# Kernel tuning notes

Measured on AMD Instinct MI355X. Metric: run time of the kernel, lower is better.

The kernel has to match this reference:

```python
import jax, jax.numpy as jnp
from jax import lax
import numpy as np

STATE_DIM, H, L = 38000, 32, 3
B, T = 256, 1024


def setup_inputs() -> dict:
    key = jax.random.key(0)
    ks = jax.random.split(key, 16)
    s = 1.0 / np.sqrt(H)
    inp = {
        "x": jax.random.randint(ks[0], (B, T), 0, STATE_DIM, dtype=jnp.int64)
        if jax.config.jax_enable_x64 else jax.random.randint(ks[0], (B, T), 0, STATE_DIM, dtype=jnp.int32),
        "hid": jnp.zeros((L, B, H), dtype=jnp.float32),
        "emb": jax.random.normal(ks[1], (STATE_DIM, H), dtype=jnp.float32),
        "W1": jax.random.uniform(ks[2], (H, H), minval=-s, maxval=s),
        "b1": jax.random.uniform(ks[3], (H,), minval=-s, maxval=s),
        "W2": jax.random.uniform(ks[4], (H, H), minval=-s, maxval=s),
        "b2": jax.random.uniform(ks[5], (H,), minval=-s, maxval=s),
        "W3": jax.random.uniform(ks[6], (H, H), minval=-s, maxval=s),
        "b3": jax.random.uniform(ks[7], (H,), minval=-s, maxval=s),
        # GRU params stacked over layers: gates order (r, z, n) as in PyTorch
        "W_ih": jax.random.uniform(ks[8], (L, 3 * H, H), minval=-s, maxval=s),
        "W_hh": jax.random.uniform(ks[9], (L, 3 * H, H), minval=-s, maxval=s),
        "b_ih": jax.random.uniform(ks[10], (L, 3 * H), minval=-s, maxval=s),
        "b_hh": jax.random.uniform(ks[11], (L, 3 * H), minval=-s, maxval=s),
    }
    return inp


def _gru_layer(x_tbh, h0, W_ih, W_hh, b_ih, b_hh):
    # x_tbh: [T,B,H]; precompute input-side gates once (memory-bound GEMM)
    gi = jnp.einsum('tbh,gh->tbg', x_tbh, W_ih) + b_ih  # [T,B,3H]

    def step(h, gi_t):
        gh = h @ W_hh.T + b_hh  # [B,3H]
        i_r, i_z, i_n = jnp.split(gi_t, 3, axis=-1)
        h_r, h_z, h_n = jnp.split(gh, 3, axis=-1)
        r = jax.nn.sigmoid(i_r + h_r)
        z = jax.nn.sigmoid(i_z + h_z)
        n = jnp.tanh(i_n + r * h_n)
        h_new = (1.0 - z) * n + z * h
        return h_new, h_new

    hT, out = lax.scan(step, h0, gi)
    return out, hT  # [T,B,H], [B,H]


def reference(x, hid, emb, W1, b1, W2, b2, W3, b3, W_ih, W_hh, b_ih, b_hh):
    e = emb[x]  # [B,T,H] embedding lookup
    e = jax.nn.relu(e @ W1.T + b1)
    e = jax.nn.relu(e @ W2.T + b2)
    e = jax.nn.relu(e @ W3.T + b3)
    seq = jnp.transpose(e, (1, 0, 2))  # [T,B,H]
    h_finals = []
    for l in range(L):
        seq, hT = _gru_layer(seq, hid[l], W_ih[l], W_hh[l], b_ih[l], b_hh[l])
        h_finals.append(hT)
    out = jnp.transpose(seq, (1, 0, 2)).reshape(x.shape[0], -1)  # [B, T*H]
    return out, jnp.stack(h_finals, axis=0)
```

## Files before the change

### kernel.cpp

```cpp
#include <hip/hip_runtime.h>

#define BB 256
#define TT 1024
#define HH 32
#define SS 16
#define NBK (TT/SS)
#define NSS (NBK+9)
#define NT 1024
#define SP 32
#define GP 96


__device__ __forceinline__ float fast_rcp(float x) { return __builtin_amdgcn_rcpf(x); }
__device__ __forceinline__ float sigm(float x)     { return fast_rcp(1.f + __expf(-x)); }
__device__ __forceinline__ float tanh_fast(float x){ float e = __expf(2.f * x); return 1.f - 2.f * fast_rcp(e + 1.f); }
__device__ __forceinline__ float rlane(float v, int k) {
    return __int_as_float(__builtin_amdgcn_readlane(__float_as_int(v), k));
}

__global__ __launch_bounds__(NT, 4) void rnn_fused(
    const int*   __restrict__ xidx,
    const float* __restrict__ hid,
    const float* __restrict__ emb,
    const float* __restrict__ W1, const float* __restrict__ b1,
    const float* __restrict__ W2, const float* __restrict__ b2,
    const float* __restrict__ W3, const float* __restrict__ b3,
    const float* __restrict__ Wih,
    const float* __restrict__ Whh,
    const float* __restrict__ bih,
    const float* __restrict__ bhh,
    float*       __restrict__ out)
{
    const int b   = blockIdx.x;
    const int tid = threadIdx.x;
    const int wv  = tid >> 6;
    const int ln  = tid & 63;
    const int lo  = ln & 31;
    const int hh  = ln >> 5;

    __shared__ alignas(16) float ebuf[2][SS][SP];
    __shared__ alignas(16) float y1s [2][SS][SP];
    __shared__ alignas(16) float y2s [2][SS][SP];
    __shared__ alignas(16) float y3s [2][SS][SP];
    __shared__ alignas(16) float h0s [2][SS][SP];
    __shared__ alignas(16) float h1s [2][SS][SP];
    __shared__ alignas(16) float gib [3][2][SS][GP];

    float wA[32], wB[32];
    float biasA = 0.f, biasB = 0.f, v_h = 0.f;

    if (wv < 3) {
        const float4* pA = reinterpret_cast<const float4*>(Whh + (size_t)(wv * 96 + ln) * HH);
        const float4* pB = reinterpret_cast<const float4*>(Whh + (size_t)(wv * 96 + 64 + lo) * HH);
        #pragma unroll
        for (int i = 0; i < 8; ++i) {
            reinterpret_cast<float4*>(wA)[i] = pA[i];
            reinterpret_cast<float4*>(wB)[i] = pB[i];
        }
        biasA = bhh[wv * 96 + ln];
        biasB = bhh[wv * 96 + 64 + lo];
        if (ln < HH) v_h = hid[(size_t)(wv * BB + b) * HH + ln];
    } else if (wv < 6) {
        const int l = wv - 3;
        const float4* pA = reinterpret_cast<const float4*>(Wih + (size_t)(l * 96 + ln) * HH);
        #pragma unroll
        for (int i = 0; i < 8; ++i) reinterpret_cast<float4*>(wA)[i] = pA[i];
        biasA = bih[l * 96 + ln];
    } else if (wv < 9) {
        const int l = wv - 6;
        const float4* pA = reinterpret_cast<const float4*>(Wih + (size_t)(l * 96 + 64 + lo) * HH);
        #pragma unroll
        for (int i = 0; i < 8; ++i) reinterpret_cast<float4*>(wA)[i] = pA[i];
        biasA = bih[l * 96 + 64 + lo];
    } else if (wv < 12) {
        const float* Ws = (wv == 9) ? W1 : (wv == 10) ? W2 : W3;
        const float* bs = (wv == 9) ? b1 : (wv == 10) ? b2 : b3;
        const float4* pA = reinterpret_cast<const float4*>(Ws + (size_t)lo * HH);
        #pragma unroll
        for (int i = 0; i < 8; ++i) reinterpret_cast<float4*>(wA)[i] = pA[i];
        biasA = bs[lo];
    }
    __syncthreads();

    float* const out_seq = out + (size_t)b * TT * HH;
    float* const out_hf  = out + (size_t)BB * TT * HH;

    for (int n = 0; n < NSS; ++n) {
        if (wv < 3) {
            const int blk = n - 5 - 2 * wv;
            if (blk >= 0 && blk < NBK) {
                const int p = blk & 1;
                const float* gsrc = &gib[wv][p][0][0];
                __builtin_amdgcn_s_setprio(1);
                for (int t2 = 0; t2 < SS; ++t2) {
                    const float giA = gsrc[t2 * GP + ln];
                    const float giB = gsrc[t2 * GP + 64 + lo];
                    float a0 = biasA, a1 = 0.f, c0 = biasB, c1 = 0.f;
                    #pragma unroll
                    for (int k = 0; k < 32; k += 2) {
                        const float h0 = rlane(v_h, k), h1 = rlane(v_h, k + 1);
                        a0 = fmaf(wA[k],     h0, a0);
                        a1 = fmaf(wA[k + 1], h1, a1);
                        c0 = fmaf(wB[k],     h0, c0);
                        c1 = fmaf(wB[k + 1], h1, c1);
                    }
                    const float sA  = giA + a0 + a1;
                    const float ghB = c0 + c1;
                    const float zp  = __shfl_xor(sA, 32);
                    const float r   = sigm(sA);
                    const float z   = sigm(zp);
                    const float nn  = tanh_fast(fmaf(r, ghB, giB));
                    const float hn  = fmaf(z, v_h - nn, nn);
                    v_h = hn;
                    if (ln < HH) {
                        if (wv == 0)      h0s[p][t2][ln] = hn;
                        else if (wv == 1) h1s[p][t2][ln] = hn;
                        else out_seq[(size_t)(blk * SS + t2) * HH + ln] = hn;
                    }
                }
                __builtin_amdgcn_s_setprio(0);
            }
        } else if (wv < 6) {
            const int l   = wv - 3;
            const int blk = n - 4 - 2 * l;
            if (blk >= 0 && blk < NBK) {
                const int p = blk & 1;
                const float* xs = (l == 0) ? &y3s[p][0][0]
                                : (l == 1) ? &h0s[p][0][0]
                                           : &h1s[p][0][0];
                float* gdst = &gib[l][p][0][0];
                for (int t2 = 0; t2 < SS; ++t2) {
                    const float4* xr = reinterpret_cast<const float4*>(xs + t2 * SP);
                    float a0 = biasA, a1 = 0.f, a2 = 0.f, a3 = 0.f;
                    #pragma unroll
                    for (int j = 0; j < 8; ++j) {
                        const float4 xv = xr[j];
                        a0 = fmaf(wA[4 * j + 0], xv.x, a0);
                        a1 = fmaf(wA[4 * j + 1], xv.y, a1);
                        a2 = fmaf(wA[4 * j + 2], xv.z, a2);
                        a3 = fmaf(wA[4 * j + 3], xv.w, a3);
                    }
                    gdst[t2 * GP + ln] = (a0 + a1) + (a2 + a3);
                }
            }
        } else if (wv < 9) {
            const int l   = wv - 6;
            const int blk = n - 4 - 2 * l;
            if (blk >= 0 && blk < NBK) {
                const int p = blk & 1;
                const float* xs = (l == 0) ? &y3s[p][0][0]
                                : (l == 1) ? &h0s[p][0][0]
                                           : &h1s[p][0][0];
                float* gdst = &gib[l][p][0][0];
                for (int t2 = 0; t2 < SS / 2; ++t2) {
                    const int tt = 2 * t2 + hh;
                    const float4* xr = reinterpret_cast<const float4*>(xs + tt * SP);
                    float a0 = biasA, a1 = 0.f, a2 = 0.f, a3 = 0.f;
                    #pragma unroll
                    for (int j = 0; j < 8; ++j) {
                        const float4 xv = xr[j];
                        a0 = fmaf(wA[4 * j + 0], xv.x, a0);
                        a1 = fmaf(wA[4 * j + 1], xv.y, a1);
                        a2 = fmaf(wA[4 * j + 2], xv.z, a2);
                        a3 = fmaf(wA[4 * j + 3], xv.w, a3);
                    }
                    gdst[tt * GP + 64 + lo] = (a0 + a1) + (a2 + a3);
                }
            }
        } else if (wv < 12) {
            const int s   = wv - 9;
            const int blk = n - 1 - s;
            if (blk >= 0 && blk < NBK) {
                const int p = blk & 1;
                const float* xs = (s == 0) ? &ebuf[p][0][0]
                                : (s == 1) ? &y1s[p][0][0]
                                           : &y2s[p][0][0];
                float* dst = (s == 0) ? &y1s[p][0][0]
                           : (s == 1) ? &y2s[p][0][0]
                                      : &y3s[p][0][0];
                for (int t2 = 0; t2 < SS / 2; ++t2) {
                    const int tt = 2 * t2 + hh;
                    const float4* xr = reinterpret_cast<const float4*>(xs + tt * SP);
                    float a0 = biasA, a1 = 0.f, a2 = 0.f, a3 = 0.f;
                    #pragma unroll
                    for (int j = 0; j < 8; ++j) {
                        const float4 xv = xr[j];
                        a0 = fmaf(wA[4 * j + 0], xv.x, a0);
                        a1 = fmaf(wA[4 * j + 1], xv.y, a1);
                        a2 = fmaf(wA[4 * j + 2], xv.z, a2);
                        a3 = fmaf(wA[4 * j + 3], xv.w, a3);
                    }
                    const float y = fmaxf((a0 + a1) + (a2 + a3), 0.f);
                    dst[tt * SP + lo] = y;
                }
            }
        } else if (wv == 12) {
            if (n < NBK) {
                const int pe = n & 1, t0 = n * SS;
                #pragma unroll
                for (int k = 0; k < 2; ++k) {
                    const int task = k * 64 + ln;
                    const int row = task >> 3, qq = task & 7;
                    const int tok = xidx[b * TT + t0 + row];
                    const float4 v = *reinterpret_cast<const float4*>(emb + (size_t)tok * HH + qq * 4);
                    *reinterpret_cast<float4*>(&ebuf[pe][row][qq * 4]) = v;
                }
            }
        }
        __syncthreads();
    }

    if (wv < 3 && ln < HH)
        out_hf[(size_t)(wv * BB + b) * HH + ln] = v_h;
}

extern "C" void kernel_launch(void* const* d_in, const int* in_sizes, int n_in,
                              void* d_out, int out_size, void* d_ws, size_t ws_size,
                              hipStream_t stream) {
    const int*   x   = (const int*)  d_in[0];
    const float* hid = (const float*)d_in[1];
    const float* emb = (const float*)d_in[2];
    const float* W1  = (const float*)d_in[3];
    const float* b1  = (const float*)d_in[4];
    const float* W2  = (const float*)d_in[5];
    const float* b2  = (const float*)d_in[6];
    const float* W3  = (const float*)d_in[7];
    const float* b3  = (const float*)d_in[8];
    const float* Wih = (const float*)d_in[9];
    const float* Whh = (const float*)d_in[10];
    const float* bih = (const float*)d_in[11];
    const float* bhh = (const float*)d_in[12];

    rnn_fused<<<dim3(BB), dim3(NT), 0, stream>>>(
        x, hid, emb, W1, b1, W2, b2, W3, b3, Wih, Whh, bih, bhh, (float*)d_out);
}
```

Measured before the change: 335.5 us.

## Process two batch elements per block with interleaved recurrent chains

Each block now handles two batch sequences, and the recurrent waves advance both hidden-state chains together. The two independent FMA chains give the scheduler instruction-level parallelism to hide the latency of the serial recurrence, and the grid shrinks to 128 blocks. The stage size is halved to keep the LDS footprint the same, which doubles the number of pipeline steps and block-wide barriers. On a 256-CU device half of the CUs now sit idle, so each block's per-step latency must drop to make up for the lost parallelism.

```diff
diff --git a/kernel.cpp b/kernel.cpp
--- a/kernel.cpp
+++ b/kernel.cpp
@@ -3,12 +3,13 @@
 #define BB 256
 #define TT 1024
 #define HH 32
-#define SS 16
+#define SS 8
 #define NBK (TT/SS)
 #define NSS (NBK+9)
 #define NT 1024
 #define SP 32
 #define GP 96
+#define EPB 2
 
 
 __device__ __forceinline__ float fast_rcp(float x) { return __builtin_amdgcn_rcpf(x); }
@@ -31,23 +32,24 @@
     const float* __restrict__ bhh,
     float*       __restrict__ out)
 {
-    const int b   = blockIdx.x;
+    const int b0  = blockIdx.x * EPB;
     const int tid = threadIdx.x;
     const int wv  = tid >> 6;
     const int ln  = tid & 63;
     const int lo  = ln & 31;
     const int hh  = ln >> 5;
 
-    __shared__ alignas(16) float ebuf[2][SS][SP];
-    __shared__ alignas(16) float y1s [2][SS][SP];
-    __shared__ alignas(16) float y2s [2][SS][SP];
-    __shared__ alignas(16) float y3s [2][SS][SP];
-    __shared__ alignas(16) float h0s [2][SS][SP];
-    __shared__ alignas(16) float h1s [2][SS][SP];
-    __shared__ alignas(16) float gib [3][2][SS][GP];
+    __shared__ alignas(16) float ebuf[EPB][2][SS][SP];
+    __shared__ alignas(16) float y1s [EPB][2][SS][SP];
+    __shared__ alignas(16) float y2s [EPB][2][SS][SP];
+    __shared__ alignas(16) float y3s [EPB][2][SS][SP];
+    __shared__ alignas(16) float h0s [EPB][2][SS][SP];
+    __shared__ alignas(16) float h1s [EPB][2][SS][SP];
+    __shared__ alignas(16) float gib [3][EPB][2][SS][GP];
 
     float wA[32], wB[32];
-    float biasA = 0.f, biasB = 0.f, v_h = 0.f;
+    float biasA = 0.f, biasB = 0.f;
+    float v_h0 = 0.f, v_h1 = 0.f;
 
     if (wv < 3) {
         const float4* pA = reinterpret_cast<const float4*>(Whh + (size_t)(wv * 96 + ln) * HH);
@@ -59,7 +61,10 @@
         }
         biasA = bhh[wv * 96 + ln];
         biasB = bhh[wv * 96 + 64 + lo];
-        if (ln < HH) v_h = hid[(size_t)(wv * BB + b) * HH + ln];
+        if (ln < HH) {
+            v_h0 = hid[(size_t)(wv * BB + b0    ) * HH + ln];
+            v_h1 = hid[(size_t)(wv * BB + b0 + 1) * HH + ln];
+        }
     } else if (wv < 6) {
         const int l = wv - 3;
         const float4* pA = reinterpret_cast<const float4*>(Wih + (size_t)(l * 96 + ln) * HH);
@@ -82,40 +87,64 @@
     }
     __syncthreads();
 
-    float* const out_seq = out + (size_t)b * TT * HH;
-    float* const out_hf  = out + (size_t)BB * TT * HH;
+    float* const out_hf = out + (size_t)BB * TT * HH;
 
     for (int n = 0; n < NSS; ++n) {
         if (wv < 3) {
             const int blk = n - 5 - 2 * wv;
             if (blk >= 0 && blk < NBK) {
                 const int p = blk & 1;
-                const float* gsrc = &gib[wv][p][0][0];
+                const float* g0 = &gib[wv][0][p][0][0];
+                const float* g1 = &gib[wv][1][p][0][0];
                 __builtin_amdgcn_s_setprio(1);
                 for (int t2 = 0; t2 < SS; ++t2) {
-                    const float giA = gsrc[t2 * GP + ln];
-                    const float giB = gsrc[t2 * GP + 64 + lo];
+                    const float giA0 = g0[t2 * GP + ln];
+                    const float giB0 = g0[t2 * GP + 64 + lo];
+                    const float giA1 = g1[t2 * GP + ln];
+                    const float giB1 = g1[t2 * GP + 64 + lo];
                     float a0 = biasA, a1 = 0.f, c0 = biasB, c1 = 0.f;
+                    float d0 = biasA, d1 = 0.f, e0 = biasB, e1 = 0.f;
                     #pragma unroll
                     for (int k = 0; k < 32; k += 2) {
-                        const float h0 = rlane(v_h, k), h1 = rlane(v_h, k + 1);
-                        a0 = fmaf(wA[k],     h0, a0);
-                        a1 = fmaf(wA[k + 1], h1, a1);
-                        c0 = fmaf(wB[k],     h0, c0);
-                        c1 = fmaf(wB[k + 1], h1, c1);
-                    }
-                    const float sA  = giA + a0 + a1;
-                    const float ghB = c0 + c1;
-                    const float zp  = __shfl_xor(sA, 32);
-                    const float r   = sigm(sA);
-                    const float z   = sigm(zp);
-                    const float nn  = tanh_fast(fmaf(r, ghB, giB));
-                    const float hn  = fmaf(z, v_h - nn, nn);
-                    v_h = hn;
+                        const float h00 = rlane(v_h0, k), h01 = rlane(v_h0, k + 1);
+                        const float h10 = rlane(v_h1, k), h11 = rlane(v_h1, k + 1);
+                        a0 = fmaf(wA[k],     h00, a0);
+                        a1 = fmaf(wA[k + 1], h01, a1);
+                        c0 = fmaf(wB[k],     h00, c0);
+                        c1 = fmaf(wB[k + 1], h01, c1);
+                        d0 = fmaf(wA[k],     h10, d0);
+                        d1 = fmaf(wA[k + 1], h11, d1);
+                        e0 = fmaf(wB[k],     h10, e0);
+                        e1 = fmaf(wB[k + 1], h11, e1);
+                    }
+                    const float sA0  = giA0 + a0 + a1;
+                    const float sA1  = giA1 + d0 + d1;
+                    const float ghB0 = c0 + c1;
+                    const float ghB1 = e0 + e1;
+                    const float zp0  = __shfl_xor(sA0, 32);
+                    const float zp1  = __shfl_xor(sA1, 32);
+                    const float r0   = sigm(sA0);
+                    const float r1   = sigm(sA1);
+                    const float z0   = sigm(zp0);
+                    const float z1   = sigm(zp1);
+                    const float nn0  = tanh_fast(fmaf(r0, ghB0, giB0));
+                    const float nn1  = tanh_fast(fmaf(r1, ghB1, giB1));
+                    const float hn0  = fmaf(z0, v_h0 - nn0, nn0);
+                    const float hn1  = fmaf(z1, v_h1 - nn1, nn1);
+                    v_h0 = hn0;
+                    v_h1 = hn1;
                     if (ln < HH) {
-                        if (wv == 0)      h0s[p][t2][ln] = hn;
-                        else if (wv == 1) h1s[p][t2][ln] = hn;
-                        else out_seq[(size_t)(blk * SS + t2) * HH + ln] = hn;
+                        if (wv == 0) {
+                            h0s[0][p][t2][ln] = hn0;
+                            h0s[1][p][t2][ln] = hn1;
+                        } else if (wv == 1) {
+                            h1s[0][p][t2][ln] = hn0;
+                            h1s[1][p][t2][ln] = hn1;
+                        } else {
+                            const size_t off = (size_t)(blk * SS + t2) * HH + ln;
+                            out[(size_t)(b0    ) * TT * HH + off] = hn0;
+                            out[(size_t)(b0 + 1) * TT * HH + off] = hn1;
+                        }
                     }
                 }
                 __builtin_amdgcn_s_setprio(0);
@@ -125,22 +154,24 @@
             const int blk = n - 4 - 2 * l;
             if (blk >= 0 && blk < NBK) {
                 const int p = blk & 1;
-                const float* xs = (l == 0) ? &y3s[p][0][0]
-                                : (l == 1) ? &h0s[p][0][0]
-                                           : &h1s[p][0][0];
-                float* gdst = &gib[l][p][0][0];
-                for (int t2 = 0; t2 < SS; ++t2) {
-                    const float4* xr = reinterpret_cast<const float4*>(xs + t2 * SP);
-                    float a0 = biasA, a1 = 0.f, a2 = 0.f, a3 = 0.f;
-                    #pragma unroll
-                    for (int j = 0; j < 8; ++j) {
-                        const float4 xv = xr[j];
-                        a0 = fmaf(wA[4 * j + 0], xv.x, a0);
-                        a1 = fmaf(wA[4 * j + 1], xv.y, a1);
-                        a2 = fmaf(wA[4 * j + 2], xv.z, a2);
-                        a3 = fmaf(wA[4 * j + 3], xv.w, a3);
-                    }
-                    gdst[t2 * GP + ln] = (a0 + a1) + (a2 + a3);
+                for (int e = 0; e < EPB; ++e) {
+                    const float* xs = (l == 0) ? &y3s[e][p][0][0]
+                                    : (l == 1) ? &h0s[e][p][0][0]
+                                               : &h1s[e][p][0][0];
+                    float* gdst = &gib[l][e][p][0][0];
+                    for (int t2 = 0; t2 < SS; ++t2) {
+                        const float4* xr = reinterpret_cast<const float4*>(xs + t2 * SP);
+                        float a0 = biasA, a1 = 0.f, a2 = 0.f, a3 = 0.f;
+                        #pragma unroll
+                        for (int j = 0; j < 8; ++j) {
+                            const float4 xv = xr[j];
+                            a0 = fmaf(wA[4 * j + 0], xv.x, a0);
+                            a1 = fmaf(wA[4 * j + 1], xv.y, a1);
+                            a2 = fmaf(wA[4 * j + 2], xv.z, a2);
+                            a3 = fmaf(wA[4 * j + 3], xv.w, a3);
+                        }
+                        gdst[t2 * GP + ln] = (a0 + a1) + (a2 + a3);
+                    }
                 }
             }
         } else if (wv < 9) {
@@ -148,23 +179,25 @@
             const int blk = n - 4 - 2 * l;
             if (blk >= 0 && blk < NBK) {
                 const int p = blk & 1;
-                const float* xs = (l == 0) ? &y3s[p][0][0]
-                                : (l == 1) ? &h0s[p][0][0]
-                                           : &h1s[p][0][0];
-                float* gdst = &gib[l][p][0][0];
-                for (int t2 = 0; t2 < SS / 2; ++t2) {
-                    const int tt = 2 * t2 + hh;
-                    const float4* xr = reinterpret_cast<const float4*>(xs + tt * SP);
-                    float a0 = biasA, a1 = 0.f, a2 = 0.f, a3 = 0.f;
-                    #pragma unroll
-                    for (int j = 0; j < 8; ++j) {
-                        const float4 xv = xr[j];
-                        a0 = fmaf(wA[4 * j + 0], xv.x, a0);
-                        a1 = fmaf(wA[4 * j + 1], xv.y, a1);
-                        a2 = fmaf(wA[4 * j + 2], xv.z, a2);
-                        a3 = fmaf(wA[4 * j + 3], xv.w, a3);
-                    }
-                    gdst[tt * GP + 64 + lo] = (a0 + a1) + (a2 + a3);
+                for (int e = 0; e < EPB; ++e) {
+                    const float* xs = (l == 0) ? &y3s[e][p][0][0]
+                                    : (l == 1) ? &h0s[e][p][0][0]
+                                               : &h1s[e][p][0][0];
+                    float* gdst = &gib[l][e][p][0][0];
+                    for (int t2 = 0; t2 < SS / 2; ++t2) {
+                        const int tt = 2 * t2 + hh;
+                        const float4* xr = reinterpret_cast<const float4*>(xs + tt * SP);
+                        float a0 = biasA, a1 = 0.f, a2 = 0.f, a3 = 0.f;
+                        #pragma unroll
+                        for (int j = 0; j < 8; ++j) {
+                            const float4 xv = xr[j];
+                            a0 = fmaf(wA[4 * j + 0], xv.x, a0);
+                            a1 = fmaf(wA[4 * j + 1], xv.y, a1);
+                            a2 = fmaf(wA[4 * j + 2], xv.z, a2);
+                            a3 = fmaf(wA[4 * j + 3], xv.w, a3);
+                        }
+                        gdst[tt * GP + 64 + lo] = (a0 + a1) + (a2 + a3);
+                    }
                 }
             }
         } else if (wv < 12) {
@@ -172,26 +205,28 @@
             const int blk = n - 1 - s;
             if (blk >= 0 && blk < NBK) {
                 const int p = blk & 1;
-                const float* xs = (s == 0) ? &ebuf[p][0][0]
-                                : (s == 1) ? &y1s[p][0][0]
-                                           : &y2s[p][0][0];
-                float* dst = (s == 0) ? &y1s[p][0][0]
-                           : (s == 1) ? &y2s[p][0][0]
-                                      : &y3s[p][0][0];
-                for (int t2 = 0; t2 < SS / 2; ++t2) {
-                    const int tt = 2 * t2 + hh;
-                    const float4* xr = reinterpret_cast<const float4*>(xs + tt * SP);
-                    float a0 = biasA, a1 = 0.f, a2 = 0.f, a3 = 0.f;
-                    #pragma unroll
-                    for (int j = 0; j < 8; ++j) {
-                        const float4 xv = xr[j];
-                        a0 = fmaf(wA[4 * j + 0], xv.x, a0);
-                        a1 = fmaf(wA[4 * j + 1], xv.y, a1);
-                        a2 = fmaf(wA[4 * j + 2], xv.z, a2);
-                        a3 = fmaf(wA[4 * j + 3], xv.w, a3);
-                    }
-                    const float y = fmaxf((a0 + a1) + (a2 + a3), 0.f);
-                    dst[tt * SP + lo] = y;
+                for (int e = 0; e < EPB; ++e) {
+                    const float* xs = (s == 0) ? &ebuf[e][p][0][0]
+                                    : (s == 1) ? &y1s[e][p][0][0]
+                                               : &y2s[e][p][0][0];
+                    float* dst = (s == 0) ? &y1s[e][p][0][0]
+                               : (s == 1) ? &y2s[e][p][0][0]
+                                          : &y3s[e][p][0][0];
+                    for (int t2 = 0; t2 < SS / 2; ++t2) {
+                        const int tt = 2 * t2 + hh;
+                        const float4* xr = reinterpret_cast<const float4*>(xs + tt * SP);
+                        float a0 = biasA, a1 = 0.f, a2 = 0.f, a3 = 0.f;
+                        #pragma unroll
+                        for (int j = 0; j < 8; ++j) {
+                            const float4 xv = xr[j];
+                            a0 = fmaf(wA[4 * j + 0], xv.x, a0);
+                            a1 = fmaf(wA[4 * j + 1], xv.y, a1);
+                            a2 = fmaf(wA[4 * j + 2], xv.z, a2);
+                            a3 = fmaf(wA[4 * j + 3], xv.w, a3);
+                        }
+                        const float y = fmaxf((a0 + a1) + (a2 + a3), 0.f);
+                        dst[tt * SP + lo] = y;
+                    }
                 }
             }
         } else if (wv == 12) {
@@ -200,18 +235,22 @@
                 #pragma unroll
                 for (int k = 0; k < 2; ++k) {
                     const int task = k * 64 + ln;
-                    const int row = task >> 3, qq = task & 7;
-                    const int tok = xidx[b * TT + t0 + row];
+                    const int e   = task >> 6;
+                    const int row = (task >> 3) & 7;
+                    const int qq  = task & 7;
+                    const int tok = xidx[(size_t)(b0 + e) * TT + t0 + row];
                     const float4 v = *reinterpret_cast<const float4*>(emb + (size_t)tok * HH + qq * 4);
-                    *reinterpret_cast<float4*>(&ebuf[pe][row][qq * 4]) = v;
+                    *reinterpret_cast<float4*>(&ebuf[e][pe][row][qq * 4]) = v;
                 }
             }
         }
         __syncthreads();
     }
 
-    if (wv < 3 && ln < HH)
-        out_hf[(size_t)(wv * BB + b) * HH + ln] = v_h;
+    if (wv < 3 && ln < HH) {
+        out_hf[(size_t)(wv * BB + b0    ) * HH + ln] = v_h0;
+        out_hf[(size_t)(wv * BB + b0 + 1) * HH + ln] = v_h1;
+    }
 }
 
 extern "C" void kernel_launch(void* const* d_in, const int* in_sizes, int n_in,
@@ -231,6 +270,6 @@
     const float* bih = (const float*)d_in[11];
     const float* bhh = (const float*)d_in[12];
 
-    rnn_fused<<<dim3(BB), dim3(NT), 0, stream>>>(
+    rnn_fused<<<dim3(BB / EPB), dim3(NT), 0, stream>>>(
         x, hid, emb, W1, b1, W2, b2, W3, b3, Wih, Whh, bih, bhh, (float*)d_out);
 }
```

Result: slower. 534.6 us (+59.3%).
